# Optimization experiments

Hardware: AMD Instinct MI355X
Metric: run time of the kernel (lower is better)

Reference implementation:

```python
import jax, jax.numpy as jnp
import numpy as np

# SLAYER neuron/simulation constants (netParams)
THETA = 10.0      # spike threshold
TAU_SR = 10.0     # PSP (SRM alpha) time constant
TAU_REF = 1.0     # refractory time constant
TAU_RHO = 1.0     # surrogate-gradient width
SCALE_RHO = 1.0   # surrogate-gradient scale
TS = 1.0          # simulation timestep
K_EPS = 100       # truncated FIR length of the alpha PSP kernel
REF_DECAY = float(np.exp(-TS / TAU_REF))


@jax.custom_vjp
def _spike_fn(v):
    # heaviside threshold with SLAYER-style exponential surrogate gradient
    return (v >= 0.0).astype(v.dtype)

def _spike_fwd(v):
    return (v >= 0.0).astype(v.dtype), v

def _spike_bwd(v, g):
    return (g * (SCALE_RHO / TAU_RHO) * jnp.exp(-jnp.abs(v) / TAU_RHO),)

_spike_fn.defvjp(_spike_fwd, _spike_bwd)


def psp(x):
    """Causal temporal filter with SRM alpha kernel eps(t)=(t/tau)exp(1-t/tau)."""
    shp = x.shape
    T = shp[-1]
    t = jnp.arange(K_EPS, dtype=x.dtype) * TS
    eps = (t / TAU_SR) * jnp.exp(1.0 - t / TAU_SR)
    xr = x.reshape(-1, 1, T)  # [N,1,T]
    y = jax.lax.conv_general_dilated(xr, eps[::-1].reshape(1, 1, K_EPS), (1,), [(K_EPS - 1, 0)])
    return y.reshape(shp)


def spike(u):
    """Sequential threshold with decaying refractory state (scan over time)."""
    uT = jnp.moveaxis(u, -1, 0)  # [T, ...]

    def step(r, u_t):
        s = _spike_fn(u_t + r - THETA)
        return REF_DECAY * r - 2.0 * THETA * s, s

    _, sT = jax.lax.scan(step, jnp.zeros(uT.shape[1:], uT.dtype), uT)
    return jnp.moveaxis(sT, 0, -1)


def pool(x, k):
    # SLAYER pool: fixed-weight sum conv, weight = 1.1*theta/(k*k) per element
    B, C, H, W, T = x.shape
    return x.reshape(B, C, H // k, k, W // k, k, T).sum(axis=(3, 5)) * (1.1 * THETA / (k * k))


def conv(x, w, pad):
    # 3D conv with time-pointwise kernel == per-timestep 2D conv (fold T into batch)
    B, C, H, W, T = x.shape
    xr = jnp.moveaxis(x, -1, 1).reshape(B * T, C, H, W)
    y = jax.lax.conv_general_dilated(xr, w, (1, 1), [(pad, pad), (pad, pad)])
    return jnp.moveaxis(y.reshape(B, T, w.shape[0], H, W), 1, -1)


def delay(x, d):
    """Per-channel learnable temporal delay via linear interpolation gather."""
    T = x.shape[-1]
    C = d.shape[0]
    t = jnp.arange(T, dtype=x.dtype)
    src = t[None, :] - d[:, None]            # [C, T]
    i0 = jnp.floor(src)
    w = (src - i0).reshape((1, C, 1, 1, T))
    i0 = i0.astype(jnp.int32)

    def take(idx):
        v = jnp.take_along_axis(x, jnp.clip(idx, 0, T - 1).reshape((1, C, 1, 1, T)), axis=-1)
        ok = ((idx >= 0) & (idx < T)).reshape((1, C, 1, 1, T))
        return jnp.where(ok, v, 0.0)

    return take(i0) * (1.0 - w) + take(i0 + 1) * w


def setup_inputs() -> dict:
    key = jax.random.key(0)
    ks = jax.random.split(key, 9)
    B, T = 4, 300
    spikeInput = (jax.random.uniform(ks[0], (B, 2, 128, 128, T)) < 0.03).astype(jnp.float32)
    conv1_w = jax.random.normal(ks[1], (16, 2, 5, 5), jnp.float32) * (1.0 / np.sqrt(2 * 25))
    conv2_w = jax.random.normal(ks[2], (32, 16, 3, 3), jnp.float32) * (1.0 / np.sqrt(16 * 9))
    fc1_w = jax.random.normal(ks[3], (512, 2048), jnp.float32) * (1.0 / np.sqrt(2048))
    fc2_w = jax.random.normal(ks[4], (11, 512), jnp.float32) * (1.0 / np.sqrt(512))
    delay1_d = jax.random.uniform(ks[5], (16,), jnp.float32) * 4.0
    delay2_d = jax.random.uniform(ks[6], (32,), jnp.float32) * 4.0
    delay3_d = jax.random.uniform(ks[7], (512,), jnp.float32) * 4.0
    return {"spikeInput": spikeInput, "conv1_w": conv1_w, "conv2_w": conv2_w,
            "fc1_w": fc1_w, "fc2_w": fc2_w,
            "delay1_d": delay1_d, "delay2_d": delay2_d, "delay3_d": delay3_d}


def reference(spikeInput, conv1_w, conv2_w, fc1_w, fc2_w, delay1_d, delay2_d, delay3_d):
    s = spike(pool(psp(spikeInput), 4))          # [B,2,32,32,T]
    s = spike(conv(psp(s), conv1_w, 2))          # [B,16,32,32,T]
    s = delay(s, delay1_d)
    s = spike(pool(psp(s), 2))                   # [B,16,16,16,T]
    s = spike(conv(psp(s), conv2_w, 1))          # [B,32,16,16,T]
    s = delay(s, delay2_d)
    s = spike(pool(psp(s), 2))                   # [B,32,8,8,T]
    B, C, H, W, T = s.shape
    s = s.reshape(B, C * H * W, 1, 1, T)         # [B,2048,1,1,T]
    s = spike(jnp.einsum('oi,bixyt->boxyt', fc1_w, psp(s)))  # [B,512,1,1,T]
    s = delay(s, delay3_d)
    s = spike(jnp.einsum('oi,bixyt->boxyt', fc2_w, psp(s)))  # [B,11,1,1,T]
    return s
```

## Files before the change

kernel.cpp:

```cpp
#include <hip/hip_runtime.h>

#define TLEN 300
#define THETA 10.0f
#define REF_DECAY 0.36787944117144233f

#define R_ 0.9048374180359595732
#define C_ 0.2718281828459045235
#define R100_ 4.5399929762484852e-05
#define RF_ ((float)R_)
#define CR100F_ ((float)(C_ * R100_))
#define C100R100F_ ((float)(100.0 * C_ * R100_))

__global__ void eps_init_kernel(float* __restrict__ eps) {
  int k = threadIdx.x;
  if (k < 104) eps[k] = 0.f;
  if (k < 100) {
    float a = (float)k / 10.0f;
    eps[k] = a * expf(1.0f - a);
  }
}

#define PSPSUB(XA, XB, YO)                                                              \
  {                                                                                     \
    QA1 = R_ * (QA1 + PA1); PA1 = R_ * PA1 + (double)(XA);                              \
    QB1 = RF_ * (QB1 + PB1); PB1 = RF_ * PB1 + (XB);                                    \
    float u = (float)(C_ * QA1) - (CR100F_ * QB1 + C100R100F_ * PB1);                   \
    float v = u + ref - THETA;                                                          \
    float sp = (v >= 0.f) ? 1.f : 0.f;                                                  \
    ref = REF_DECAY * ref - 20.0f * sp;                                                 \
    h3 = (h3 << 1) | (h2 >> 31); h2 = (h2 << 1) | (h1 >> 31);                           \
    h1 = (h1 << 1) | (h0 >> 31); h0 = (h0 << 1) | (unsigned)sp;                         \
    float spb = (float)((h3 >> 4) & 1u);                                                \
    QA2 = R_ * (QA2 + PA2); PA2 = R_ * PA2 + (double)sp;                                \
    QB2 = RF_ * (QB2 + PB2); PB2 = RF_ * PB2 + spb;                                     \
    YO = (float)(C_ * QA2) - (CR100F_ * QB2 + C100R100F_ * PB2);                        \
  }

__global__ __launch_bounds__(64) void psp_spike_psp_scan_kernel(const float* __restrict__ in,
                                                                float* __restrict__ out,
                                                                long rows) {
  long row = (long)blockIdx.x * 64 + threadIdx.x;
  if (row >= rows) return;
  const float* xr = in + row * TLEN;
  float* yr = out + row * TLEN;
  double PA1 = 0, QA1 = 0, PA2 = 0, QA2 = 0;
  float PB1 = 0.f, QB1 = 0.f, PB2 = 0.f, QB2 = 0.f;
  float ref = 0.f;
  unsigned h0 = 0, h1 = 0, h2 = 0, h3 = 0;
#pragma unroll 1
  for (int tq = 0; tq < 75; ++tq) {
    const int t = 4 * tq;
    const float4 xa = *reinterpret_cast<const float4*>(xr + t);
    float4 xb = make_float4(0.f, 0.f, 0.f, 0.f);
    if (t >= 100) xb = *reinterpret_cast<const float4*>(xr + t - 100);
    float4 yo;
    PSPSUB(xa.x, xb.x, yo.x);
    PSPSUB(xa.y, xb.y, yo.y);
    PSPSUB(xa.z, xb.z, yo.z);
    PSPSUB(xa.w, xb.w, yo.w);
    *reinterpret_cast<float4*>(yr + t) = yo;
  }
}

__global__ __launch_bounds__(256) void pool4_kernel(const float* __restrict__ in,
                                                    float* __restrict__ out) {
  int idx = blockIdx.x * 256 + threadIdx.x;
  if (idx >= 153600) return;
  int tq = idx % 75;
  int rest = idx / 75;
  int x = rest & 31; rest >>= 5;
  int y = rest & 31; rest >>= 5;
  const float* base = in + ((long)(rest * 128 + y * 4) * 128 + x * 4) * TLEN + tq * 4;
  float4 s = {0.f, 0.f, 0.f, 0.f};
#pragma unroll
  for (int dy = 0; dy < 4; ++dy)
#pragma unroll
    for (int dx = 0; dx < 4; ++dx) {
      float4 v = *reinterpret_cast<const float4*>(base + (dy * 128 + dx) * TLEN);
      s.x += v.x; s.y += v.y; s.z += v.z; s.w += v.w;
    }
  s.x *= 0.6875f; s.y *= 0.6875f; s.z *= 0.6875f; s.w *= 0.6875f;
  *reinterpret_cast<float4*>(out + ((long)(rest * 32 + y) * 32 + x) * TLEN + tq * 4) = s;
}

#define FIRSTEP(e, A, B, C)                                                              \
  acc[0] += e.x * B.x; acc[1] += e.x * B.y; acc[2] += e.x * B.z; acc[3] += e.x * B.w;    \
  acc[4] += e.x * C.x; acc[5] += e.x * C.y; acc[6] += e.x * C.z; acc[7] += e.x * C.w;    \
  acc[0] += e.y * A.w; acc[1] += e.y * B.x; acc[2] += e.y * B.y; acc[3] += e.y * B.z;    \
  acc[4] += e.y * B.w; acc[5] += e.y * C.x; acc[6] += e.y * C.y; acc[7] += e.y * C.z;    \
  acc[0] += e.z * A.z; acc[1] += e.z * A.w; acc[2] += e.z * B.x; acc[3] += e.z * B.y;    \
  acc[4] += e.z * B.z; acc[5] += e.z * B.w; acc[6] += e.z * C.x; acc[7] += e.z * C.y;    \
  acc[0] += e.w * A.y; acc[1] += e.w * A.z; acc[2] += e.w * A.w; acc[3] += e.w * B.x;    \
  acc[4] += e.w * B.y; acc[5] += e.w * B.z; acc[6] += e.w * B.w; acc[7] += e.w * C.x;

__device__ __forceinline__ float4 ldq(const float* __restrict__ rowp, int w) {
  if (w >= 0 && w < TLEN) return *reinterpret_cast<const float4*>(rowp + w);
  return make_float4(0.f, 0.f, 0.f, 0.f);
}

__global__ __launch_bounds__(256) void fir_direct_kernel(const float* __restrict__ in,
                                                         float* __restrict__ out,
                                                         const float* __restrict__ epsg,
                                                         int rows) {
  int task = blockIdx.x * 256 + threadIdx.x;
  int row = task / 38;
  int l = task - row * 38;
  if (row >= rows) return;
  const float* rowp = in + (long)row * TLEN;
  const int t0 = 8 * l;
  float4 A = ldq(rowp, t0 - 4);
  float4 B = ldq(rowp, t0);
  float4 C = ldq(rowp, t0 + 4);
  float acc[8];
#pragma unroll
  for (int j = 0; j < 8; ++j) acc[j] = 0.f;
#pragma unroll 1
  for (int kg0 = 0; kg0 < 80; kg0 += 20) {
    const float* ep = epsg + kg0;
#pragma unroll
    for (int kk = 0; kk < 5; ++kk) {
      const float4 e = *reinterpret_cast<const float4*>(ep + 4 * kk);
      const int kg = kg0 + 4 * kk;
      FIRSTEP(e, A, B, C);
      C = B; B = A;
      A = ldq(rowp, t0 - kg - 8);
    }
    __builtin_amdgcn_sched_barrier(0);
  }
#pragma unroll
  for (int kk = 0; kk < 5; ++kk) {
    const float4 e = *reinterpret_cast<const float4*>(epsg + 80 + 4 * kk);
    FIRSTEP(e, A, B, C);
    C = B; B = A;
    if (kk < 4) A = ldq(rowp, t0 - 88 - 4 * kk);
  }
  float* op = out + (long)row * TLEN + t0;
  *reinterpret_cast<float4*>(op) = make_float4(acc[0], acc[1], acc[2], acc[3]);
  if (t0 + 4 < TLEN)
    *reinterpret_cast<float4*>(op + 4) = make_float4(acc[4], acc[5], acc[6], acc[7]);
}

__global__ __launch_bounds__(64) void scan_reduce4_kernel(const float* __restrict__ part,
                                                          float* __restrict__ s) {
  long row = (long)blockIdx.x * 64 + threadIdx.x;
  const float* p = part + row * TLEN;
  float* o = s + row * TLEN;
  float ref = 0.f;
#pragma unroll 4
  for (int c4 = 0; c4 < 75; ++c4) {
    const float4 v0 = *reinterpret_cast<const float4*>(p + 4 * c4);
    const float4 v1 = *reinterpret_cast<const float4*>(p + 614400 + 4 * c4);
    const float4 v2 = *reinterpret_cast<const float4*>(p + 1228800 + 4 * c4);
    const float4 v3 = *reinterpret_cast<const float4*>(p + 1843200 + 4 * c4);
    float4 u4;
    u4.x = (v0.x + v1.x) + (v2.x + v3.x);
    u4.y = (v0.y + v1.y) + (v2.y + v3.y);
    u4.z = (v0.z + v1.z) + (v2.z + v3.z);
    u4.w = (v0.w + v1.w) + (v2.w + v3.w);
    float v, sp;
    v = u4.x + ref - THETA; sp = (v >= 0.f) ? 1.f : 0.f; u4.x = sp; ref = REF_DECAY * ref - 20.0f * sp;
    v = u4.y + ref - THETA; sp = (v >= 0.f) ? 1.f : 0.f; u4.y = sp; ref = REF_DECAY * ref - 20.0f * sp;
    v = u4.z + ref - THETA; sp = (v >= 0.f) ? 1.f : 0.f; u4.z = sp; ref = REF_DECAY * ref - 20.0f * sp;
    v = u4.w + ref - THETA; sp = (v >= 0.f) ? 1.f : 0.f; u4.w = sp; ref = REF_DECAY * ref - 20.0f * sp;
    *reinterpret_cast<float4*>(o + 4 * c4) = u4;
  }
}

__global__ __launch_bounds__(256) void delay_kernel(const float* __restrict__ in,
                                                    const float* __restrict__ d,
                                                    float* __restrict__ out, int total) {
  int idx = blockIdx.x * 256 + threadIdx.x;
  if (idx >= total) return;
  int t = idx % TLEN;
  int rest = idx / TLEN;
  float dd = d[rest & 511];
  float src = (float)t - dd;
  float fi = floorf(src);
  int i0 = (int)fi;
  float wf = src - fi;
  const float* base = in + (long)rest * TLEN;
  float v0 = (i0 >= 0 && i0 < TLEN) ? base[min(max(i0, 0), TLEN - 1)] : 0.f;
  float v1 = (i0 + 1 >= 0 && i0 + 1 < TLEN) ? base[min(max(i0 + 1, 0), TLEN - 1)] : 0.f;
  out[idx] = v0 * (1.f - wf) + v1 * wf;
}

__device__ __forceinline__ int sqz(int r, int q) { return (q & ~7) | ((q + r) & 7); }

__global__ __launch_bounds__(256) void spike_pool2_delay_kernel(const float* __restrict__ u,
                                                                const float* __restrict__ dly,
                                                                float* __restrict__ out,
                                                                int WI, int C) {
  __shared__ float4 ch[64 * 16];
  __shared__ unsigned int bits[64 * 13];
  const int tid = threadIdx.x;
  const long inrow0 = (long)blockIdx.x * 64;
  float ref = 0.f;
  unsigned int wbits = 0;
  for (int cix = 0; cix < 5; ++cix) {
    __syncthreads();
    for (int i = tid; i < 960; i += 256) {
      int r = i / 15, q = i - r * 15;
      ch[r * 16 + sqz(r, q)] = *reinterpret_cast<const float4*>(
          u + (inrow0 + r) * TLEN + cix * 60 + 4 * q);
    }
    __syncthreads();
    if (tid < 64) {
      int r = tid;
#pragma unroll 1
      for (int q = 0; q < 15; ++q) {
        float4 v = ch[r * 16 + sqz(r, q)];
        int t = cix * 60 + 4 * q;
        float x, sp;
        x = v.x + ref - THETA; sp = (x >= 0.f) ? 1.f : 0.f; ref = REF_DECAY * ref - 20.0f * sp;
        wbits |= ((unsigned int)sp) << (t & 31);
        if ((t & 31) == 31) { bits[r * 13 + (t >> 5)] = wbits; wbits = 0; }
        x = v.y + ref - THETA; sp = (x >= 0.f) ? 1.f : 0.f; ref = REF_DECAY * ref - 20.0f * sp;
        wbits |= ((unsigned int)sp) << ((t + 1) & 31);
        if (((t + 1) & 31) == 31) { bits[r * 13 + ((t + 1) >> 5)] = wbits; wbits = 0; }
        x = v.z + ref - THETA; sp = (x >= 0.f) ? 1.f : 0.f; ref = REF_DECAY * ref - 20.0f * sp;
        wbits |= ((unsigned int)sp) << ((t + 2) & 31);
        if (((t + 2) & 31) == 31) { bits[r * 13 + ((t + 2) >> 5)] = wbits; wbits = 0; }
        x = v.w + ref - THETA; sp = (x >= 0.f) ? 1.f : 0.f; ref = REF_DECAY * ref - 20.0f * sp;
        wbits |= ((unsigned int)sp) << ((t + 3) & 31);
        if (((t + 3) & 31) == 31) { bits[r * 13 + ((t + 3) >> 5)] = wbits; wbits = 0; }
      }
    }
  }
  if (tid < 64) bits[tid * 13 + 9] = wbits;
  __syncthreads();
  const int WO = WI >> 1;
  const int bc = (int)(inrow0 / (WI * WI));
  const int y0 = (int)((inrow0 % (WI * WI)) / WI);
  const float dd = dly[bc % C];
  const long orow0 = (long)bc * (WO * WO) + (y0 >> 1) * WO;
  for (int i = tid; i < 4800; i += 256) {
    int ro = i / TLEN, t = i - ro * TLEN;
    int Yr = ro / WO, X = ro - Yr * WO;
    int ir = (2 * Yr) * WI + 2 * X;
    float src = (float)t - dd;
    float fi = floorf(src);
    int i0 = (int)fi;
    float wf = src - fi;
    bool ok0 = (i0 >= 0) && (i0 < TLEN);
    bool ok1 = (i0 + 1 >= 0) && (i0 + 1 < TLEN);
    int j0 = min(max(i0, 0), TLEN - 1);
    int j1 = min(max(i0 + 1, 0), TLEN - 1);
    int s0i = 0, s1i = 0;
#pragma unroll
    for (int dy = 0; dy < 2; ++dy)
#pragma unroll
      for (int dx = 0; dx < 2; ++dx) {
        int rr = ir + dy * WI + dx;
        s0i += (int)((bits[rr * 13 + (j0 >> 5)] >> (j0 & 31)) & 1u);
        s1i += (int)((bits[rr * 13 + (j1 >> 5)] >> (j1 & 31)) & 1u);
      }
    float s0 = ok0 ? (float)s0i : 0.f;
    float s1 = ok1 ? (float)s1i : 0.f;
    out[(orow0 + ro) * TLEN + t] = (s0 * (1.f - wf) + s1 * wf) * 2.75f;
  }
}

__global__ __launch_bounds__(256) void conv1_kernel(const float* __restrict__ in,
                                                    const float* __restrict__ w,
                                                    float* __restrict__ out) {
  __shared__ float xl[11520];
  const int tid = threadIdx.x;
  const int t0 = blockIdx.x * 32;
  const int y = blockIdx.y;
  const int b = blockIdx.z;
  for (int i = tid; i < 2880; i += 256) {
    int tq = i & 7;
    int rest = i >> 3;
    int xp = rest % 36;
    int r2 = rest / 36;
    int dy = r2 % 5;
    int c = r2 / 5;
    int yy = y + dy - 2, xx = xp - 2, t = t0 + tq * 4;
    float4 v = {0.f, 0.f, 0.f, 0.f};
    if (yy >= 0 && yy < 32 && xx >= 0 && xx < 32 && t < TLEN)
      v = *reinterpret_cast<const float4*>(
          in + ((long)((b * 2 + c) * 32 + yy) * 32 + xx) * TLEN + t);
    *reinterpret_cast<float4*>(&xl[rest * 32 + tq * 4]) = v;
  }
  __syncthreads();
  const int tg = tid & 7;
  const int x = tid >> 3;
  float acc[16][4];
#pragma unroll
  for (int o = 0; o < 16; ++o) { acc[o][0] = acc[o][1] = acc[o][2] = acc[o][3] = 0.f; }
  for (int c = 0; c < 2; ++c)
#pragma unroll
    for (int dy = 0; dy < 5; ++dy)
#pragma unroll
      for (int kx = 0; kx < 5; ++kx) {
        const float4 xv = *reinterpret_cast<const float4*>(
            &xl[((c * 5 + dy) * 36 + x + kx) * 32 + tg * 4]);
        const float* wp = w + (c * 5 + dy) * 5 + kx;
#pragma unroll
        for (int o = 0; o < 16; ++o) {
          float wsc = wp[o * 50];
          acc[o][0] += wsc * xv.x; acc[o][1] += wsc * xv.y;
          acc[o][2] += wsc * xv.z; acc[o][3] += wsc * xv.w;
        }
      }
  const int t = t0 + tg * 4;
  if (t < TLEN) {
#pragma unroll
    for (int o = 0; o < 16; ++o) {
      float4 res; res.x = acc[o][0]; res.y = acc[o][1]; res.z = acc[o][2]; res.w = acc[o][3];
      *reinterpret_cast<float4*>(&out[((long)((b * 16 + o) * 32 + y) * 32 + x) * TLEN + t]) = res;
    }
  }
}

__global__ __launch_bounds__(256) void conv2_kernel(const float* __restrict__ in,
                                                    const float* __restrict__ w,
                                                    float* __restrict__ out) {
  __shared__ float xl[13824];
  const int tid = threadIdx.x;
  const int t0 = blockIdx.x * 16;
  const int y = blockIdx.y;
  const int b = blockIdx.z;
  for (int i = tid; i < 3456; i += 256) {
    int tq = i & 3;
    int rest = i >> 2;
    int xp = rest % 18;
    int r2 = rest / 18;
    int dy = r2 % 3;
    int c = r2 / 3;
    int yy = y + dy - 1, xx = xp - 1, t = t0 + tq * 4;
    float4 v = {0.f, 0.f, 0.f, 0.f};
    if (yy >= 0 && yy < 16 && xx >= 0 && xx < 16 && t < TLEN)
      v = *reinterpret_cast<const float4*>(
          in + ((long)((b * 16 + c) * 16 + yy) * 16 + xx) * TLEN + t);
    *reinterpret_cast<float4*>(&xl[rest * 16 + tq * 4]) = v;
  }
  __syncthreads();
  const int tg = tid & 3;
  const int x = (tid >> 2) & 15;
  const int oh = tid >> 6;
  float acc[8][4];
#pragma unroll
  for (int o = 0; o < 8; ++o) { acc[o][0] = acc[o][1] = acc[o][2] = acc[o][3] = 0.f; }
  for (int c = 0; c < 16; ++c)
#pragma unroll
    for (int dy = 0; dy < 3; ++dy)
#pragma unroll
      for (int kx = 0; kx < 3; ++kx) {
        const float4 xv = *reinterpret_cast<const float4*>(
            &xl[((c * 3 + dy) * 18 + x + kx) * 16 + tg * 4]);
        const float* wp = w + (c * 3 + dy) * 3 + kx;
#pragma unroll
        for (int oo = 0; oo < 8; ++oo) {
          float wsc = wp[(oh * 8 + oo) * 144];
          acc[oo][0] += wsc * xv.x; acc[oo][1] += wsc * xv.y;
          acc[oo][2] += wsc * xv.z; acc[oo][3] += wsc * xv.w;
        }
      }
  const int t = t0 + tg * 4;
  if (t < TLEN) {
#pragma unroll
    for (int oo = 0; oo < 8; ++oo) {
      int o = oh * 8 + oo;
      float4 res; res.x = acc[oo][0]; res.y = acc[oo][1]; res.z = acc[oo][2]; res.w = acc[oo][3];
      *reinterpret_cast<float4*>(&out[((long)((b * 32 + o) * 16 + y) * 16 + x) * TLEN + t]) = res;
    }
  }
}

__global__ __launch_bounds__(256) void fc1_kernel(const float* __restrict__ x,
                                                  const float* __restrict__ w,
                                                  float* __restrict__ part) {
  __shared__ float wl[64][44];
  __shared__ float xlb[32][68];
  const int tid = threadIdx.x;
  const int t0 = blockIdx.x * 64;
  const int o0 = blockIdx.y * 64;
  const int b = blockIdx.z >> 2;
  const int split = blockIdx.z & 3;
  const int tx = tid & 15, ty = tid >> 4;
  float acc[4][4];
#pragma unroll
  for (int i = 0; i < 4; ++i)
#pragma unroll
    for (int j = 0; j < 4; ++j) acc[i][j] = 0.f;
  const int kbeg = split * 512;
  for (int kc = kbeg; kc < kbeg + 512; kc += 32) {
    __syncthreads();
#pragma unroll
    for (int rr = 0; rr < 2; ++rr) {
      int i = rr * 256 + tid;
      int ol = i >> 3, kq = i & 7;
      float4 v = *reinterpret_cast<const float4*>(w + (long)(o0 + ol) * 2048 + kc + kq * 4);
      *reinterpret_cast<float4*>(&wl[ol][kq * 4]) = v;
    }
#pragma unroll
    for (int rr = 0; rr < 2; ++rr) {
      int i = rr * 256 + tid;
      int kl = i >> 4, tq = i & 15;
      int t = t0 + tq * 4;
      float4 v = {0.f, 0.f, 0.f, 0.f};
      if (t < TLEN)
        v = *reinterpret_cast<const float4*>(x + ((long)b * 2048 + kc + kl) * TLEN + t);
      *reinterpret_cast<float4*>(&xlb[kl][tq * 4]) = v;
    }
    __syncthreads();
#pragma unroll
    for (int k4 = 0; k4 < 8; ++k4) {
      float4 wq[4], xq[4];
#pragma unroll
      for (int i = 0; i < 4; ++i)
        wq[i] = *reinterpret_cast<const float4*>(&wl[ty * 4 + i][k4 * 4]);
#pragma unroll
      for (int j = 0; j < 4; ++j)
        xq[j] = *reinterpret_cast<const float4*>(&xlb[k4 * 4 + j][tx * 4]);
#pragma unroll
      for (int i = 0; i < 4; ++i) {
        float wa[4] = {wq[i].x, wq[i].y, wq[i].z, wq[i].w};
#pragma unroll
        for (int j = 0; j < 4; ++j) {
          float xa[4] = {xq[j].x, xq[j].y, xq[j].z, xq[j].w};
          acc[i][0] += wa[j] * xa[0]; acc[i][1] += wa[j] * xa[1];
          acc[i][2] += wa[j] * xa[2]; acc[i][3] += wa[j] * xa[3];
        }
      }
    }
  }
  const int t = t0 + tx * 4;
  if (t < TLEN) {
#pragma unroll
    for (int i = 0; i < 4; ++i) {
      float4 res; res.x = acc[i][0]; res.y = acc[i][1]; res.z = acc[i][2]; res.w = acc[i][3];
      *reinterpret_cast<float4*>(
          part + ((long)(split * 4 + b) * 512 + o0 + ty * 4 + i) * TLEN + t) = res;
    }
  }
}

__global__ __launch_bounds__(320) void fc2_spike_kernel(const float* __restrict__ x,
                                                        const float* __restrict__ w,
                                                        float* __restrict__ out) {
  __shared__ float ul[304];
  int blk = blockIdx.x;
  int b = blk / 11, o = blk % 11;
  int t = threadIdx.x;
  if (t < TLEN) {
    const float* xr = x + (long)b * 512 * TLEN + t;
    const float* wr = w + o * 512;
    float a0 = 0.f, a1 = 0.f, a2 = 0.f, a3 = 0.f;
#pragma unroll 4
    for (int i = 0; i < 512; i += 4) {
      a0 += wr[i] * xr[(long)i * TLEN];
      a1 += wr[i + 1] * xr[(long)(i + 1) * TLEN];
      a2 += wr[i + 2] * xr[(long)(i + 2) * TLEN];
      a3 += wr[i + 3] * xr[(long)(i + 3) * TLEN];
    }
    ul[t] = (a0 + a1) + (a2 + a3);
  }
  __syncthreads();
  if (t == 0) {
    float ref = 0.f;
#pragma unroll 4
    for (int c = 0; c < TLEN; ++c) {
      float v = ul[c] + ref - THETA;
      float sp = (v >= 0.f) ? 1.f : 0.f;
      ul[c] = sp;
      ref = REF_DECAY * ref - 20.0f * sp;
    }
  }
  __syncthreads();
  if (t < TLEN) out[((long)b * 11 + o) * TLEN + t] = ul[t];
}

extern "C" void kernel_launch(void* const* d_in, const int* in_sizes, int n_in,
                              void* d_out, int out_size, void* d_ws, size_t ws_size,
                              hipStream_t stream) {
  const float* input = (const float*)d_in[0];
  const float* w1    = (const float*)d_in[1];
  const float* w2    = (const float*)d_in[2];
  const float* wfc1  = (const float*)d_in[3];
  const float* wfc2  = (const float*)d_in[4];
  const float* d1    = (const float*)d_in[5];
  const float* d2    = (const float*)d_in[6];
  const float* d3    = (const float*)d_in[7];

  float* ws   = (float*)d_ws;
  float* big0 = ws;
  float* medA = big0 + 19660800;
  float* medB = medA + 4915200;
  float* fcA  = medB + 4915200;
  float* fcB  = fcA + 614400;
  float* eps  = fcB + 614400;

  hipLaunchKernelGGL(eps_init_kernel, dim3(1), dim3(128), 0, stream, eps);

  hipLaunchKernelGGL(pool4_kernel, dim3(600), dim3(256), 0, stream, input, medA);
  hipLaunchKernelGGL(psp_spike_psp_scan_kernel, dim3(128), dim3(64), 0, stream,
                     medA, medB, 8192L);
  hipLaunchKernelGGL(conv1_kernel, dim3(10, 32, 4), dim3(256), 0, stream, medB, w1, big0);
  hipLaunchKernelGGL(spike_pool2_delay_kernel, dim3(1024), dim3(256), 0, stream,
                     big0, d1, medA, 32, 16);
  hipLaunchKernelGGL(psp_spike_psp_scan_kernel, dim3(256), dim3(64), 0, stream,
                     medA, medB, 16384L);
  hipLaunchKernelGGL(conv2_kernel, dim3(19, 16, 4), dim3(256), 0, stream, medB, w2, big0);
  hipLaunchKernelGGL(spike_pool2_delay_kernel, dim3(512), dim3(256), 0, stream,
                     big0, d2, medA, 16, 32);
  hipLaunchKernelGGL(psp_spike_psp_scan_kernel, dim3(128), dim3(64), 0, stream,
                     medA, medB, 8192L);
  hipLaunchKernelGGL(fc1_kernel, dim3(5, 8, 16), dim3(256), 0, stream, medB, wfc1, big0);
  hipLaunchKernelGGL(scan_reduce4_kernel, dim3(32), dim3(64), 0, stream, big0, fcA);
  hipLaunchKernelGGL(delay_kernel, dim3(2400), dim3(256), 0, stream, fcA, d3, fcB, 614400);
  hipLaunchKernelGGL(fir_direct_kernel, dim3(304), dim3(256), 0, stream, fcB, fcA, eps, 2048);
  hipLaunchKernelGGL(fc2_spike_kernel, dim3(44), dim3(320), 0, stream, fcA, wfc2, (float*)d_out);
}
```

Measured before the change: 443.0 us.

## Stage PSP scan input rows through LDS ring buffer with coalesced loads

The fused psp-spike-psp scan kernel now has its 64 threads cooperatively load 64 input rows into shared memory in 60-sample chunks. Each row lives in a 240-float ring buffer, and the next chunk is prefetched while the current one is scanned. Each thread then reads its current samples and its 100-step-delayed samples from LDS instead of making strided per-row global loads. This is meant to coalesce the global reads, but it uses about 62 KB of LDS per 64-thread block, which can cap occupancy severely, and it drops the row bound check.

Result: no change. 451.7 us (+2.0%).

```diff
diff --git a/kernel.cpp b/kernel.cpp
--- a/kernel.cpp
+++ b/kernel.cpp
@@ -36,29 +36,53 @@
     YO = (float)(C_ * QA2) - (CR100F_ * QB2 + C100R100F_ * PB2);                        \
   }
 
+#define RSTRIDE 244
 __global__ __launch_bounds__(64) void psp_spike_psp_scan_kernel(const float* __restrict__ in,
                                                                 float* __restrict__ out,
                                                                 long rows) {
-  long row = (long)blockIdx.x * 64 + threadIdx.x;
-  if (row >= rows) return;
-  const float* xr = in + row * TLEN;
-  float* yr = out + row * TLEN;
+  __shared__ float xs[64 * RSTRIDE];
+  const int tid = threadIdx.x;
+  const long row0 = (long)blockIdx.x * 64;
+  for (int i = tid; i < 960; i += 64) {
+    int rr = i / 15, q = i - rr * 15;
+    *reinterpret_cast<float4*>(&xs[rr * RSTRIDE + 4 * q]) =
+        *reinterpret_cast<const float4*>(in + (row0 + rr) * TLEN + 4 * q);
+  }
+  const int r = tid;
+  float* yr = out + (row0 + r) * TLEN;
+  const float* myrow = &xs[r * RSTRIDE];
   double PA1 = 0, QA1 = 0, PA2 = 0, QA2 = 0;
   float PB1 = 0.f, QB1 = 0.f, PB2 = 0.f, QB2 = 0.f;
   float ref = 0.f;
   unsigned h0 = 0, h1 = 0, h2 = 0, h3 = 0;
 #pragma unroll 1
-  for (int tq = 0; tq < 75; ++tq) {
-    const int t = 4 * tq;
-    const float4 xa = *reinterpret_cast<const float4*>(xr + t);
-    float4 xb = make_float4(0.f, 0.f, 0.f, 0.f);
-    if (t >= 100) xb = *reinterpret_cast<const float4*>(xr + t - 100);
-    float4 yo;
-    PSPSUB(xa.x, xb.x, yo.x);
-    PSPSUB(xa.y, xb.y, yo.y);
-    PSPSUB(xa.z, xb.z, yo.z);
-    PSPSUB(xa.w, xb.w, yo.w);
-    *reinterpret_cast<float4*>(yr + t) = yo;
+  for (int c = 0; c < 5; ++c) {
+    if (c + 1 < 5) {
+      const int gbase = 60 * (c + 1);
+      const int rbase = (gbase >= 240) ? gbase - 240 : gbase;
+      for (int i = tid; i < 960; i += 64) {
+        int rr = i / 15, q = i - rr * 15;
+        *reinterpret_cast<float4*>(&xs[rr * RSTRIDE + rbase + 4 * q]) =
+            *reinterpret_cast<const float4*>(in + (row0 + rr) * TLEN + gbase + 4 * q);
+      }
+    }
+    __syncthreads();
+    const int rp = (c == 4) ? 0 : 60 * c;
+#pragma unroll 1
+    for (int tq = 0; tq < 15; ++tq) {
+      const int t = 60 * c + 4 * tq;
+      const float4 xa = *reinterpret_cast<const float4*>(myrow + rp + 4 * tq);
+      float4 xb = make_float4(0.f, 0.f, 0.f, 0.f);
+      if (t >= 100)
+        xb = *reinterpret_cast<const float4*>(myrow + (t - 100));
+      float4 yo;
+      PSPSUB(xa.x, xb.x, yo.x);
+      PSPSUB(xa.y, xb.y, yo.y);
+      PSPSUB(xa.z, xb.z, yo.z);
+      PSPSUB(xa.w, xb.w, yo.w);
+      *reinterpret_cast<float4*>(yr + t) = yo;
+    }
+    __syncthreads();
   }
 }
 
```
